# Kernel optimization log

Measured on AMD Instinct MI355X. Metric: run time of the kernel, lower is better.

The kernel has to match this reference:

```python
import jax, jax.numpy as jnp
import numpy as np

L1 = 3072
L2 = 15
L3 = 32
COUNT = 8
KAN_G = 3   # grid intervals
KAN_K = 3   # spline order


def _bspline_basis(x, grid, k):
    """Cox-de Boor B-spline basis. x: [B, in], grid: [in, G+2k+1] -> [B, in, G+k]."""
    x = x[:, :, None]                      # [B, in, 1]
    g = grid[None]                         # [1, in, M]
    B0 = ((x >= g[:, :, :-1]) & (x < g[:, :, 1:])).astype(x.dtype)
    for d in range(1, k + 1):
        B0 = ((x - g[:, :, : -(d + 1)]) / (g[:, :, d:-1] - g[:, :, : -(d + 1)]) * B0[:, :, :-1]
              + (g[:, :, d + 1:] - x) / (g[:, :, d + 1:] - g[:, :, 1:-d]) * B0[:, :, 1:])
    return B0  # [B, in, G+k]


def setup_inputs() -> dict:
    key = jax.random.key(0)
    ks = jax.random.split(key, 9)
    B = 16384
    in_dim = L2 * 2            # 30
    out_dim = L3 * COUNT       # 256
    x = jax.random.normal(ks[0], (B, L1), jnp.float32) * 0.1
    ls_indices = jax.random.randint(ks[1], (B,), 0, COUNT, dtype=jnp.int32)
    l1_w = jax.random.normal(ks[2], ((L2 + 1) * COUNT, L1), jnp.float32) / np.sqrt(L1).astype(np.float32)
    l1_b = jax.random.normal(ks[3], ((L2 + 1) * COUNT,), jnp.float32) * 0.01
    l1f_w = jax.random.normal(ks[4], (L2 + 1, L1), jnp.float32) / np.sqrt(L1).astype(np.float32)
    l1f_b = jnp.zeros((L2 + 1,), jnp.float32)
    # KAN layer: uniform extended grid on [-1,1], G+2k+1 = 10 knots per input dim
    h = 2.0 / KAN_G
    g1 = jnp.arange(-KAN_K, KAN_G + KAN_K + 1, dtype=jnp.float32) * h - 1.0
    kan_grid = jnp.tile(g1[None], (in_dim, 1))                      # [30, 10]
    kan_coef = jax.random.normal(ks[5], (in_dim, out_dim, KAN_G + KAN_K), jnp.float32) * 0.1
    kan_scale_base = jax.random.normal(ks[6], (in_dim, out_dim), jnp.float32) / np.sqrt(in_dim).astype(np.float32)
    kan_scale_sp = jnp.ones((in_dim, out_dim), jnp.float32)
    out_w = jax.random.normal(ks[7], (COUNT, L3), jnp.float32) / np.sqrt(L3).astype(np.float32)
    out_b = jnp.zeros((COUNT,), jnp.float32)
    return dict(x=x, ls_indices=ls_indices, l1_w=l1_w, l1_b=l1_b, l1f_w=l1f_w, l1f_b=l1f_b,
                kan_grid=kan_grid, kan_coef=kan_coef, kan_scale_base=kan_scale_base,
                kan_scale_sp=kan_scale_sp, out_w=out_w, out_b=out_b)


def reference(x, ls_indices, l1_w, l1_b, l1f_w, l1f_b, kan_grid, kan_coef,
              kan_scale_base, kan_scale_sp, out_w, out_b):
    B = x.shape[0]
    idx = ls_indices.reshape(-1) + jnp.arange(B, dtype=ls_indices.dtype) * COUNT  # [B]
    # l1: dense over all stacks, then gather the selected stack row per sample
    l1s = (x @ l1_w.T + l1_b).reshape(B * COUNT, L2 + 1)
    l1c = l1s[idx]                                  # [B, L2+1]
    l1f = x @ l1f_w.T + l1f_b                       # [B, L2+1]
    l1c_, l1c_out = l1c[:, :L2], l1c[:, L2:]
    l1f_, l1f_out = l1f[:, :L2], l1f[:, L2:]
    l1x = l1c_ + l1f_                               # [B, L2]
    l1x = jnp.clip(jnp.concatenate([l1x * l1x * (127.0 / 128.0), l1x], axis=1), 0.0, 1.0)  # [B, 2*L2]
    # KAN layer (single KANLayer, 30 -> 256): silu base + B-spline, summed over inputs
    basis = _bspline_basis(l1x, kan_grid, KAN_K)    # [B, 30, G+k]
    w_sp = kan_coef * kan_scale_sp[:, :, None]      # fold scale into coef -> [30, 256, G+k]
    l2s = (jnp.einsum('bi,io->bo', jax.nn.silu(l1x), kan_scale_base)
           + jnp.einsum('bik,iok->bo', basis, w_sp))  # [B, 256]
    l2c = l2s.reshape(B * COUNT, L3)[idx]           # [B, L3]
    l2x = jnp.clip(l2c, 0.0, 1.0)
    l3s = (l2x @ out_w.T + out_b).reshape(B * COUNT, 1)
    l3c = l3s[idx]                                  # [B, 1]
    return l3c + l1f_out + l1c_out
```

## Files before the change

### kernel.cpp

```cpp
#include <hip/hip_runtime.h>
#include <hip/hip_bf16.h>
#include <math.h>

#define NB 16384
#define KD 3072
#define TPB 256
#define CAP 2560
#define K2B 64
#define BPB 160

typedef __attribute__((ext_vector_type(8))) short bf16x8;
typedef __attribute__((ext_vector_type(4))) float f32x4;

#define WS_W_OFF 82048
#define WS_WK_OFF 966784

__device__ __forceinline__ unsigned short f2bf(float f) {
    unsigned u = __float_as_uint(f);
    u += 0x7FFFu + ((u >> 16) & 1u);
    return (unsigned short)(u >> 16);
}

__device__ __forceinline__ unsigned pk2(float a, float b) {
    float2 t; t.x = a; t.y = b;
    __hip_bfloat162 h = __float22bfloat162_rn(t);
    return *(unsigned*)&h;
}

__global__ void k_pre(const float* __restrict__ l1_w, const float* __restrict__ l1f_w,
                      unsigned short* __restrict__ W,
                      const float* __restrict__ coef, const float* __restrict__ sb,
                      const float* __restrict__ sp, unsigned short* __restrict__ Wk,
                      const int* __restrict__ ls, int* __restrict__ meta) {
    int bid = blockIdx.x;
    int tid = threadIdx.x;
    if (bid < 432) {
        int g = bid * TPB + tid;
        int e = g * 4;
        const float* src = (e < 128 * KD) ? (l1_w + e) : (l1f_w + (e - 128 * KD));
        float4 v = *(const float4*)src;
        int2 o;
        o.x = (unsigned)f2bf(v.x) | ((unsigned)f2bf(v.y) << 16);
        o.y = (unsigned)f2bf(v.z) | ((unsigned)f2bf(v.w) << 16);
        *(int2*)(W + e) = o;
    } else if (bid < 688) {
        int o = bid - 432;
        int k = tid;
        if (k < 224) {
            float val = 0.f;
            if (k < 30) {
                val = sb[k * 256 + o];
            } else if (k >= 32 && k < 212) {
                int t = k - 32;
                int i = t / 6;
                int kk = t - i * 6;
                val = coef[((size_t)i * 256 + o) * 6 + kk] * sp[i * 256 + o];
            }
            Wk[o * 224 + k] = f2bf(val);
        }
    } else {
        int j = bid - 688;
        int r = j * TPB + tid;
        int bb = ls[r];
        int lane = tid & 63;
        int* idxL = meta + 16;
        for (int qq = 0; qq < 8; qq++) {
            unsigned long long mask = __ballot(bb == qq);
            if (mask != 0ull) {
                int leader = __ffsll((unsigned long long)mask) - 1;
                int base = 0;
                if (lane == leader) base = atomicAdd(&meta[qq], (int)__popcll(mask));
                base = __shfl(base, leader);
                if (bb == qq) {
                    int rank = (int)__popcll(mask & ((1ull << lane) - 1ull));
                    int pos = base + rank;
                    if (pos < CAP) idxL[qq * CAP + pos] = r;
                }
            }
        }
    }
}

__global__ __launch_bounds__(K2B, 2) void k2_main(
    const float* __restrict__ x, const int* __restrict__ meta,
    const unsigned short* __restrict__ W, const unsigned short* __restrict__ Wk,
    const float* __restrict__ l1_b, const float* __restrict__ l1f_b,
    const float* __restrict__ out_w, const float* __restrict__ out_b,
    float* __restrict__ out)
{
    __shared__ float hS[16][33];
    __shared__ unsigned short uL[16][232];

    int tid = threadIdx.x;
    int q = blockIdx.x / BPB;
    int rel0 = (blockIdx.x - q * BPB) * 16;
    int cnt = meta[q]; if (cnt > CAP) cnt = CAP;
    if (rel0 >= cnt) return;
    const int* idxL = meta + 16;
    int myrow = 0, myvalid = 0;
    if (tid < 16) {
        int rel = rel0 + tid;
        myvalid = (rel < cnt) ? 1 : 0;
        myrow = idxL[q * CAP + (myvalid ? rel : 0)];
    }
    int l16 = tid & 15, quad = tid >> 4;
    int arow = __shfl(myrow, l16);

    const float* aP = x + (size_t)arow * KD + quad * 8;
    const unsigned short* b0P = W + (size_t)(q * 16 + l16) * KD + quad * 8;
    const unsigned short* b1P = W + (size_t)(128 + l16) * KD + quad * 8;

    f32x4 acc0 = {0.f, 0.f, 0.f, 0.f};
    f32x4 acc1 = {0.f, 0.f, 0.f, 0.f};

    float4 ca[8]; int4 cb0[4], cb1[4];
    float4 na[8]; int4 nb0[4], nb1[4];
#pragma unroll
    for (int s = 0; s < 4; s++) {
        ca[2 * s]     = *(const float4*)(aP + s * 32);
        ca[2 * s + 1] = *(const float4*)(aP + s * 32 + 4);
        cb0[s] = *(const int4*)(b0P + s * 32);
        cb1[s] = *(const int4*)(b1P + s * 32);
    }
    for (int kt = 0; kt < 24; kt += 2) {
        {
            const float* ap = aP + (kt + 1) * 128;
            const unsigned short* p0 = b0P + (kt + 1) * 128;
            const unsigned short* p1 = b1P + (kt + 1) * 128;
#pragma unroll
            for (int s = 0; s < 4; s++) {
                na[2 * s]     = *(const float4*)(ap + s * 32);
                na[2 * s + 1] = *(const float4*)(ap + s * 32 + 4);
                nb0[s] = *(const int4*)(p0 + s * 32);
                nb1[s] = *(const int4*)(p1 + s * 32);
            }
        }
#pragma unroll
        for (int s = 0; s < 4; s++) {
            int4 ai;
            ai.x = pk2(ca[2 * s].x, ca[2 * s].y);
            ai.y = pk2(ca[2 * s].z, ca[2 * s].w);
            ai.z = pk2(ca[2 * s + 1].x, ca[2 * s + 1].y);
            ai.w = pk2(ca[2 * s + 1].z, ca[2 * s + 1].w);
            bf16x8 af = *(bf16x8*)&ai;
            acc0 = __builtin_amdgcn_mfma_f32_16x16x32_bf16(af, *(bf16x8*)&cb0[s], acc0, 0, 0, 0);
            acc1 = __builtin_amdgcn_mfma_f32_16x16x32_bf16(af, *(bf16x8*)&cb1[s], acc1, 0, 0, 0);
        }
        if (kt < 22) {
            const float* ap = aP + (kt + 2) * 128;
            const unsigned short* p0 = b0P + (kt + 2) * 128;
            const unsigned short* p1 = b1P + (kt + 2) * 128;
#pragma unroll
            for (int s = 0; s < 4; s++) {
                ca[2 * s]     = *(const float4*)(ap + s * 32);
                ca[2 * s + 1] = *(const float4*)(ap + s * 32 + 4);
                cb0[s] = *(const int4*)(p0 + s * 32);
                cb1[s] = *(const int4*)(p1 + s * 32);
            }
        }
#pragma unroll
        for (int s = 0; s < 4; s++) {
            int4 ai;
            ai.x = pk2(na[2 * s].x, na[2 * s].y);
            ai.y = pk2(na[2 * s].z, na[2 * s].w);
            ai.z = pk2(na[2 * s + 1].x, na[2 * s + 1].y);
            ai.w = pk2(na[2 * s + 1].z, na[2 * s + 1].w);
            bf16x8 af = *(bf16x8*)&ai;
            acc0 = __builtin_amdgcn_mfma_f32_16x16x32_bf16(af, *(bf16x8*)&nb0[s], acc0, 0, 0, 0);
            acc1 = __builtin_amdgcn_mfma_f32_16x16x32_bf16(af, *(bf16x8*)&nb1[s], acc1, 0, 0, 0);
        }
    }

    {
        float bsel = l1_b[q * 16 + l16];
        float bff  = l1f_b[l16];
#pragma unroll
        for (int r = 0; r < 4; r++) {
            hS[quad * 4 + r][l16]      = acc0[r] + bsel;
            hS[quad * 4 + r][16 + l16] = acc1[r] + bff;
        }
    }
    __syncthreads();

#pragma unroll
    for (int t = 0; t < 4; t++) {
        int it = tid + 64 * t;
        if (it < 240) {
            int i = it >> 4;
            int m = it & 15;
            float v = hS[m][i] + hS[m][16 + i];
            float xs = fminf(v * v * (127.f / 128.f), 1.f);
            float xl = fminf(fmaxf(v, 0.f), 1.f);
#pragma unroll
            for (int which = 0; which < 2; which++) {
                float xv = which ? xl : xs;
                int ii = which ? (15 + i) : i;
                float sg = 1.f / (1.f + __expf(-xv));
                uL[m][ii] = f2bf(xv * sg);
                float s = xv * 1.5f + 4.5f;
                int j = (int)s;
                float f = s - (float)j;
                float omf = 1.f - f;
                float f2 = f * f, f3 = f2 * f;
                float N0 = omf * omf * omf * (1.f / 6.f);
                float N1 = (3.f * f3 - 6.f * f2 + 4.f) * (1.f / 6.f);
                float N2 = (-3.f * f3 + 3.f * f2 + 3.f * f + 1.f) * (1.f / 6.f);
                float N3 = f3 * (1.f / 6.f);
                float b1 = (j == 4) ? N0 : 0.f;
                float b2 = (j == 4) ? N1 : ((j == 5) ? N0 : 0.f);
                float b3 = (j == 4) ? N2 : ((j == 5) ? N1 : N0);
                float b4 = (j == 4) ? N3 : ((j == 5) ? N2 : N1);
                float b5 = (j == 5) ? N3 : ((j == 6) ? N2 : 0.f);
                unsigned* dst = (unsigned*)&uL[m][32 + ii * 6];
                dst[0] = ((unsigned)f2bf(b1) << 16);
                dst[1] = (unsigned)f2bf(b2) | ((unsigned)f2bf(b3) << 16);
                dst[2] = (unsigned)f2bf(b4) | ((unsigned)f2bf(b5) << 16);
            }
        }
    }
    if (tid < 16) {
        *(unsigned*)&uL[tid][30] = 0;
        unsigned* z = (unsigned*)&uL[tid][212];
        z[0] = 0; z[1] = 0; z[2] = 0; z[3] = 0; z[4] = 0; z[5] = 0;
    }
    __syncthreads();

    f32x4 acc2a = {0.f, 0.f, 0.f, 0.f};
    f32x4 acc2b = {0.f, 0.f, 0.f, 0.f};
    {
        const unsigned short* uP  = &uL[l16][quad * 8];
        const unsigned short* k0P = Wk + (size_t)(q * 32 + l16) * 224 + quad * 8;
        const unsigned short* k1P = Wk + (size_t)(q * 32 + 16 + l16) * 224 + quad * 8;
#pragma unroll
        for (int ks = 0; ks < 7; ks++) {
            bf16x8 uf = *(const bf16x8*)(uP + ks * 32);
            acc2a = __builtin_amdgcn_mfma_f32_16x16x32_bf16(uf, *(const bf16x8*)(k0P + ks * 32), acc2a, 0, 0, 0);
            acc2b = __builtin_amdgcn_mfma_f32_16x16x32_bf16(uf, *(const bf16x8*)(k1P + ks * 32), acc2b, 0, 0, 0);
        }
    }

    float ow0 = out_w[q * 32 + l16];
    float ow1 = out_w[q * 32 + 16 + l16];
    float p[4];
#pragma unroll
    for (int r = 0; r < 4; r++) {
        p[r] = fminf(fmaxf(acc2a[r], 0.f), 1.f) * ow0
             + fminf(fmaxf(acc2b[r], 0.f), 1.f) * ow1;
    }
#pragma unroll
    for (int off = 1; off < 16; off <<= 1) {
        p[0] += __shfl_xor(p[0], off);
        p[1] += __shfl_xor(p[1], off);
        p[2] += __shfl_xor(p[2], off);
        p[3] += __shfl_xor(p[3], off);
    }
    int rowm[4], valm[4];
#pragma unroll
    for (int r = 0; r < 4; r++) {
        rowm[r] = __shfl(myrow, quad * 4 + r);
        valm[r] = __shfl(myvalid, quad * 4 + r);
    }
    if (l16 == 0) {
        float obq = out_b[q];
#pragma unroll
        for (int r = 0; r < 4; r++) {
            int m = quad * 4 + r;
            if (valm[r]) out[rowm[r]] = p[r] + obq + hS[m][15] + hS[m][31];
        }
    }
}

extern "C" void kernel_launch(void* const* d_in, const int* in_sizes, int n_in,
                              void* d_out, int out_size, void* d_ws, size_t ws_size,
                              hipStream_t stream) {
    (void)in_sizes; (void)n_in; (void)out_size; (void)ws_size;
    const float* x     = (const float*)d_in[0];
    const int*   ls    = (const int*)d_in[1];
    const float* l1_w  = (const float*)d_in[2];
    const float* l1_b  = (const float*)d_in[3];
    const float* l1f_w = (const float*)d_in[4];
    const float* l1f_b = (const float*)d_in[5];
    const float* coef  = (const float*)d_in[7];
    const float* sb    = (const float*)d_in[8];
    const float* sp    = (const float*)d_in[9];
    const float* ow    = (const float*)d_in[10];
    const float* ob    = (const float*)d_in[11];
    float* out = (float*)d_out;

    char* ws = (char*)d_ws;
    int* meta = (int*)ws;
    unsigned short* W  = (unsigned short*)(ws + WS_W_OFF);
    unsigned short* Wk = (unsigned short*)(ws + WS_WK_OFF);

    hipMemsetAsync(meta, 0, 64, stream);
    hipLaunchKernelGGL(k_pre, dim3(752), dim3(TPB), 0, stream,
                       l1_w, l1f_w, W, coef, sb, sp, Wk, ls, meta);
    hipLaunchKernelGGL(k2_main, dim3(8 * BPB), dim3(K2B), 0, stream,
                       x, meta, W, Wk, l1_b, l1f_b, ow, ob, out);
}
```

Baseline: 344.4 us.

## Replace atomic bucketing with per-block count tables and prefix-sum lookup

Per-stack sample bucketing no longer uses global atomics into a capped index list. Each preprocessing block now writes its own per-stack counts and a 256-slot index list. The main kernel rebuilds global offsets with a wavefront prefix scan and a linear search per row. This also drops the memset launch and removes the CAP truncation, so sample order within a stack is now deterministic. Bias and output-weight loads are hoisted ahead of the GEMM loop, at the cost of a scan plus a search over 64 entries in every block.

```diff
diff --git a/kernel.cpp b/kernel.cpp
--- a/kernel.cpp
+++ b/kernel.cpp
@@ -5,15 +5,15 @@
 #define NB 16384
 #define KD 3072
 #define TPB 256
-#define CAP 2560
 #define K2B 64
 #define BPB 160
 
 typedef __attribute__((ext_vector_type(8))) short bf16x8;
 typedef __attribute__((ext_vector_type(4))) float f32x4;
 
-#define WS_W_OFF 82048
-#define WS_WK_OFF 966784
+#define WS_IDX_OFF 2048
+#define WS_W_OFF 526336
+#define WS_WK_OFF 1411072
 
 __device__ __forceinline__ unsigned short f2bf(float f) {
     unsigned u = __float_as_uint(f);
@@ -31,7 +31,10 @@
                       unsigned short* __restrict__ W,
                       const float* __restrict__ coef, const float* __restrict__ sb,
                       const float* __restrict__ sp, unsigned short* __restrict__ Wk,
-                      const int* __restrict__ ls, int* __restrict__ meta) {
+                      const int* __restrict__ ls, int* __restrict__ cntTab,
+                      int* __restrict__ idxL) {
+    __shared__ int wcnt[4][8];
+    __shared__ int woff[4][8];
     int bid = blockIdx.x;
     int tid = threadIdx.x;
     if (bid < 432) {
@@ -62,27 +65,33 @@
         int j = bid - 688;
         int r = j * TPB + tid;
         int bb = ls[r];
-        int lane = tid & 63;
-        int* idxL = meta + 16;
-        for (int qq = 0; qq < 8; qq++) {
-            unsigned long long mask = __ballot(bb == qq);
-            if (mask != 0ull) {
-                int leader = __ffsll((unsigned long long)mask) - 1;
-                int base = 0;
-                if (lane == leader) base = atomicAdd(&meta[qq], (int)__popcll(mask));
-                base = __shfl(base, leader);
-                if (bb == qq) {
-                    int rank = (int)__popcll(mask & ((1ull << lane) - 1ull));
-                    int pos = base + rank;
-                    if (pos < CAP) idxL[qq * CAP + pos] = r;
-                }
-            }
-        }
+        int wv = tid >> 6, lane = tid & 63;
+        int rank = 0;
+        unsigned long long ltmask = (lane == 63) ? ~0ull : ((1ull << (lane + 1)) - 1ull);
+        ltmask >>= 1; ltmask <<= 1; ltmask = (1ull << lane) - 1ull;
+        for (int q = 0; q < 8; q++) {
+            unsigned long long mask = __ballot(bb == q);
+            if (bb == q) rank = (int)__popcll(mask & ltmask);
+            if (lane == 0) wcnt[wv][q] = (int)__popcll(mask);
+        }
+        __syncthreads();
+        if (tid < 8) {
+            int s = 0;
+#pragma unroll
+            for (int w = 0; w < 4; w++) {
+                woff[w][tid] = s;
+                s += wcnt[w][tid];
+            }
+            cntTab[j * 8 + tid] = s;
+        }
+        __syncthreads();
+        idxL[(j * 8 + bb) * 256 + woff[wv][bb] + rank] = r;
     }
 }
 
 __global__ __launch_bounds__(K2B, 2) void k2_main(
-    const float* __restrict__ x, const int* __restrict__ meta,
+    const float* __restrict__ x, const int* __restrict__ cntTab,
+    const int* __restrict__ idxL,
     const unsigned short* __restrict__ W, const unsigned short* __restrict__ Wk,
     const float* __restrict__ l1_b, const float* __restrict__ l1f_b,
     const float* __restrict__ out_w, const float* __restrict__ out_b,
@@ -90,18 +99,33 @@
 {
     __shared__ float hS[16][33];
     __shared__ unsigned short uL[16][232];
+    __shared__ int s_pre[64];
 
     int tid = threadIdx.x;
     int q = blockIdx.x / BPB;
     int rel0 = (blockIdx.x - q * BPB) * 16;
-    int cnt = meta[q]; if (cnt > CAP) cnt = CAP;
-    if (rel0 >= cnt) return;
-    const int* idxL = meta + 16;
+
+    int jcnt = cntTab[tid * 8 + q];
+    int pre = jcnt;
+#pragma unroll
+    for (int off = 1; off < 64; off <<= 1) {
+        int t = __shfl_up(pre, off);
+        if (tid >= off) pre += t;
+    }
+    int total = __shfl(pre, 63);
+    if (rel0 >= total) return;
+    s_pre[tid] = pre;
+    __syncthreads();
+
     int myrow = 0, myvalid = 0;
     if (tid < 16) {
         int rel = rel0 + tid;
-        myvalid = (rel < cnt) ? 1 : 0;
-        myrow = idxL[q * CAP + (myvalid ? rel : 0)];
+        myvalid = (rel < total) ? 1 : 0;
+        int rl = myvalid ? rel : 0;
+        int j = 0;
+        while (s_pre[j] <= rl) j++;
+        int base = j ? s_pre[j - 1] : 0;
+        myrow = idxL[(j * 8 + q) * 256 + rl - base];
     }
     int l16 = tid & 15, quad = tid >> 4;
     int arow = __shfl(myrow, l16);
@@ -109,6 +133,12 @@
     const float* aP = x + (size_t)arow * KD + quad * 8;
     const unsigned short* b0P = W + (size_t)(q * 16 + l16) * KD + quad * 8;
     const unsigned short* b1P = W + (size_t)(128 + l16) * KD + quad * 8;
+
+    float bsel = l1_b[q * 16 + l16];
+    float bff  = l1f_b[l16];
+    float ow0  = out_w[q * 32 + l16];
+    float ow1  = out_w[q * 32 + 16 + l16];
+    float obq  = out_b[q];
 
     f32x4 acc0 = {0.f, 0.f, 0.f, 0.f};
     f32x4 acc1 = {0.f, 0.f, 0.f, 0.f};
@@ -171,14 +201,10 @@
         }
     }
 
-    {
-        float bsel = l1_b[q * 16 + l16];
-        float bff  = l1f_b[l16];
-#pragma unroll
-        for (int r = 0; r < 4; r++) {
-            hS[quad * 4 + r][l16]      = acc0[r] + bsel;
-            hS[quad * 4 + r][16 + l16] = acc1[r] + bff;
-        }
+#pragma unroll
+    for (int r = 0; r < 4; r++) {
+        hS[quad * 4 + r][l16]      = acc0[r] + bsel;
+        hS[quad * 4 + r][16 + l16] = acc1[r] + bff;
     }
     __syncthreads();
 
@@ -239,8 +265,6 @@
         }
     }
 
-    float ow0 = out_w[q * 32 + l16];
-    float ow1 = out_w[q * 32 + 16 + l16];
     float p[4];
 #pragma unroll
     for (int r = 0; r < 4; r++) {
@@ -261,7 +285,6 @@
         valm[r] = __shfl(myvalid, quad * 4 + r);
     }
     if (l16 == 0) {
-        float obq = out_b[q];
 #pragma unroll
         for (int r = 0; r < 4; r++) {
             int m = quad * 4 + r;
@@ -288,13 +311,13 @@
     float* out = (float*)d_out;
 
     char* ws = (char*)d_ws;
-    int* meta = (int*)ws;
+    int* cntTab = (int*)ws;
+    int* idxL   = (int*)(ws + WS_IDX_OFF);
     unsigned short* W  = (unsigned short*)(ws + WS_W_OFF);
     unsigned short* Wk = (unsigned short*)(ws + WS_WK_OFF);
 
-    hipMemsetAsync(meta, 0, 64, stream);
     hipLaunchKernelGGL(k_pre, dim3(752), dim3(TPB), 0, stream,
-                       l1_w, l1f_w, W, coef, sb, sp, Wk, ls, meta);
+                       l1_w, l1f_w, W, coef, sb, sp, Wk, ls, cntTab, idxL);
     hipLaunchKernelGGL(k2_main, dim3(8 * BPB), dim3(K2B), 0, stream,
-                       x, meta, W, Wk, l1_b, l1f_b, ow, ob, out);
-}
+                       x, cntTab, idxL, W, Wk, l1_b, l1f_b, ow, ob, out);
+}
```

Measured after the change: 317.3 us. -7.9%, faster.
